# Performance work log

Measured on AMD Instinct MI355X. Metric: run time of the kernel, lower is better.

Reference implementation:

```python
import jax, jax.numpy as jnp
import numpy as np

NUM_SEGMENTS = 16

def setup_inputs() -> dict:
    key = jax.random.key(0)
    k1, k2, k3, k4 = jax.random.split(key, 4)
    C, R = 256, 4
    x = jax.random.normal(k1, (1000000, C), dtype=jnp.float32)
    indices = jax.random.randint(k2, (1000000,), 0, NUM_SEGMENTS, dtype=jnp.int64)
    # Linear weights (torch Linear: y = x @ W.T); store as (in, out) for einsum
    w1 = jax.random.normal(k3, (C, C // R), dtype=jnp.float32) / np.sqrt(C)
    w2 = jax.random.normal(k4, (C // R, C), dtype=jnp.float32) / np.sqrt(C // R)
    return {"x": x, "indices": indices, "w1": w1, "w2": w2}

def reference(x, indices, w1, w2):
    idx = indices.astype(jnp.int32)
    # scatter-mean over segments: (S, C)
    seg_sum = jax.ops.segment_sum(x, idx, num_segments=NUM_SEGMENTS)
    counts = jax.ops.segment_sum(jnp.ones((x.shape[0],), x.dtype), idx, num_segments=NUM_SEGMENTS)
    seg_mean = seg_sum / jnp.maximum(counts, 1.0)[:, None]
    # tiny SE MLP: Linear -> ReLU -> Linear -> Sigmoid
    h = jax.nn.relu(seg_mean @ w1)
    gate = jax.nn.sigmoid(h @ w2)  # (S, C)
    # gather per-point gate and modulate
    return x * gate[idx]
```

## Files before the change

### kernel.cpp

```cpp
#include <hip/hip_runtime.h>
#include <math.h>

#define C 256
#define S 16
#define CR 64
#define NREP 16

__global__ __launch_bounds__(256) void k_hist(
    const int* __restrict__ idx, int* __restrict__ pcnt, int nrows)
{
    const int lane = threadIdx.x & 63;
    const int tid  = blockIdx.x * blockDim.x + threadIdx.x;
    const int T    = gridDim.x * blockDim.x;
    const int padded = ((nrows + 63) >> 6) << 6;

    int c0=0,c1=0,c2=0,c3=0,c4=0,c5=0,c6=0,c7=0,
        c8=0,c9=0,c10=0,c11=0,c12=0,c13=0,c14=0,c15=0;

    for (int i = tid; i < padded; i += T) {
        const int v = (i < nrows) ? idx[i] : -1;
        #define CNT(K) c##K += (int)__popcll(__ballot(v == K));
        CNT(0)  CNT(1)  CNT(2)  CNT(3)  CNT(4)  CNT(5)  CNT(6)  CNT(7)
        CNT(8)  CNT(9)  CNT(10) CNT(11) CNT(12) CNT(13) CNT(14) CNT(15)
        #undef CNT
    }
    if (lane == 0) {
        #define FL(K) if (c##K) atomicAdd(&pcnt[K], c##K);
        FL(0)  FL(1)  FL(2)  FL(3)  FL(4)  FL(5)  FL(6)  FL(7)
        FL(8)  FL(9)  FL(10) FL(11) FL(12) FL(13) FL(14) FL(15)
        #undef FL
    }
}

__global__ __launch_bounds__(256, 2) void k_segsum(
    const float* __restrict__ x, const int* __restrict__ idx,
    float* __restrict__ psum, int nrows)
{
    const int lane = threadIdx.x & 63;
    const int w    = threadIdx.x >> 6;
    const int gw   = blockIdx.x * 4 + w;
    const int nw   = gridDim.x * 4;

    float4 a0={0,0,0,0},a1={0,0,0,0},a2={0,0,0,0},a3={0,0,0,0},
           a4={0,0,0,0},a5={0,0,0,0},a6={0,0,0,0},a7={0,0,0,0},
           a8={0,0,0,0},a9={0,0,0,0},a10={0,0,0,0},a11={0,0,0,0},
           a12={0,0,0,0},a13={0,0,0,0},a14={0,0,0,0},a15={0,0,0,0};

    const float4* __restrict__ x4 = reinterpret_cast<const float4*>(x);

    #define ACC1(K, sv, vv) { const float m = (sv == K) ? 1.0f : 0.0f; \
        a##K.x = fmaf(m, vv.x, a##K.x); a##K.y = fmaf(m, vv.y, a##K.y); \
        a##K.z = fmaf(m, vv.z, a##K.z); a##K.w = fmaf(m, vv.w, a##K.w); }
    #define ROW(sv, vv) \
        ACC1(0,sv,vv)  ACC1(1,sv,vv)  ACC1(2,sv,vv)  ACC1(3,sv,vv) \
        ACC1(4,sv,vv)  ACC1(5,sv,vv)  ACC1(6,sv,vv)  ACC1(7,sv,vv) \
        ACC1(8,sv,vv)  ACC1(9,sv,vv)  ACC1(10,sv,vv) ACC1(11,sv,vv) \
        ACC1(12,sv,vv) ACC1(13,sv,vv) ACC1(14,sv,vv) ACC1(15,sv,vv)

    const int nbatch = nrows >> 2;
    for (int b = gw; b < nbatch; b += nw) {
        const int r = b << 2;
        const int s0 = __builtin_amdgcn_readfirstlane(idx[r + 0]);
        const int s1 = __builtin_amdgcn_readfirstlane(idx[r + 1]);
        const int s2 = __builtin_amdgcn_readfirstlane(idx[r + 2]);
        const int s3 = __builtin_amdgcn_readfirstlane(idx[r + 3]);
        const float4* __restrict__ p = x4 + (size_t)r * (C/4) + lane;
        const float4 v0 = p[0 * (C/4)];
        const float4 v1 = p[1 * (C/4)];
        const float4 v2 = p[2 * (C/4)];
        const float4 v3 = p[3 * (C/4)];
        ROW(s0, v0) ROW(s1, v1) ROW(s2, v2) ROW(s3, v3)
    }
    if (gw == 0) {
        for (int r = nbatch << 2; r < nrows; ++r) {
            const int s = __builtin_amdgcn_readfirstlane(idx[r]);
            const float4 v = x4[(size_t)r * (C/4) + lane];
            ROW(s, v)
        }
    }
    #undef ROW
    #undef ACC1

    __shared__ float red[4][S][C];
    #define ST(K) *reinterpret_cast<float4*>(&red[w][K][4 * lane]) = a##K;
    ST(0)  ST(1)  ST(2)  ST(3)  ST(4)  ST(5)  ST(6)  ST(7)
    ST(8)  ST(9)  ST(10) ST(11) ST(12) ST(13) ST(14) ST(15)
    #undef ST
    __syncthreads();

    const int t   = threadIdx.x;
    const int rep = blockIdx.x & (NREP - 1);
    float* gs = psum + (size_t)rep * S * C;
    #pragma unroll
    for (int s_ = 0; s_ < S; s_++) {
        const float v = red[0][s_][t] + red[1][s_][t] +
                        red[2][s_][t] + red[3][s_][t];
        atomicAdd(&gs[s_ * C + t], v);
    }
}

__global__ __launch_bounds__(256) void k_mlp(
    const float* __restrict__ psum, const int* __restrict__ pcnt,
    const float* __restrict__ w1, const float* __restrict__ w2,
    float* __restrict__ gate)
{
    __shared__ float sm[S][C];
    __shared__ float h[S][CR];
    __shared__ float cnt[S];
    const int t = threadIdx.x;

    if (t < S) cnt[t] = fmaxf((float)pcnt[t], 1.0f);
    __syncthreads();

    for (int i = t; i < S * C; i += 256) {
        float v = 0.0f;
        #pragma unroll
        for (int r = 0; r < NREP; r++) v += psum[r * S * C + i];
        sm[i / C][i % C] = v / cnt[i / C];
    }
    __syncthreads();

    for (int o = t; o < S * CR; o += 256) {
        const int s = o / CR, j = o % CR;
        float acc = 0.0f;
        #pragma unroll 4
        for (int k = 0; k < C; k++) acc += sm[s][k] * w1[k * CR + j];
        h[s][j] = fmaxf(acc, 0.0f);
    }
    __syncthreads();

    for (int o = t; o < S * C; o += 256) {
        const int s = o / C, j = o % C;
        float acc = 0.0f;
        #pragma unroll
        for (int k = 0; k < CR; k++) acc += h[s][k] * w2[k * C + j];
        gate[o] = 1.0f / (1.0f + expf(-acc));
    }
}

__global__ __launch_bounds__(256) void k_mod(
    const float* __restrict__ x, const int* __restrict__ idx,
    const float* __restrict__ gate, float* __restrict__ out, int nrows)
{
    const int l    = threadIdx.x & 63;
    const int wrow = threadIdx.x >> 6;
    const float4* __restrict__ x4 = reinterpret_cast<const float4*>(x);
    const float4* __restrict__ g4 = reinterpret_cast<const float4*>(gate);
    float4* __restrict__ o4 = reinterpret_cast<float4*>(out);

    for (int row = blockIdx.x * 4 + wrow; row < nrows; row += gridDim.x * 4) {
        const int s = idx[row];
        float4 v = x4[row * (C / 4) + l];
        const float4 g = g4[s * (C / 4) + l];
        v.x *= g.x; v.y *= g.y; v.z *= g.z; v.w *= g.w;
        o4[row * (C / 4) + l] = v;
    }
}

extern "C" void kernel_launch(void* const* d_in, const int* in_sizes, int n_in,
                              void* d_out, int out_size, void* d_ws, size_t ws_size,
                              hipStream_t stream)
{
    const float* x   = (const float*)d_in[0];
    const int*   idx = (const int*)  d_in[1];
    const float* w1  = (const float*)d_in[2];
    const float* w2  = (const float*)d_in[3];
    float* out = (float*)d_out;
    const int nrows = in_sizes[1];

    float* psum = (float*)d_ws;
    int*   pcnt = (int*)(psum + NREP * S * C);
    float* gate = (float*)(pcnt + S);

    const size_t zero_bytes = NREP * S * C * sizeof(float) + S * sizeof(int);
    hipMemsetAsync(d_ws, 0, zero_bytes, stream);

    k_hist  <<<  64, 256, 0, stream>>>(idx, pcnt, nrows);
    k_segsum<<<1024, 256, 0, stream>>>(x, idx, psum, nrows);
    k_mlp   <<<   1, 256, 0, stream>>>(psum, pcnt, w1, w2, gate);
    k_mod   <<<2048, 256, 0, stream>>>(x, idx, gate, out, nrows);
}
```

Baseline: 740.2 us.

## Batch rows per wave with lane-broadcast indices and nontemporal loads/stores

Both the segment-sum and modulate kernels now give each wave a 64-row superblock. The wave loads all 64 indices with one coalesced load and broadcasts each one with readlane, and it issues several row loads at a time as nontemporal accesses to raise memory-level parallelism. The segsum kernel halves its shared reduction buffer by reducing in two 8-segment passes and raises its occupancy hint to 4 blocks per SM. The histogram grid doubles. More waves per SM may raise register pressure or cause spills with 64 accumulator floats, and nontemporal loads keep x out of cache between the two passes.

```diff
diff --git a/kernel.cpp b/kernel.cpp
--- a/kernel.cpp
+++ b/kernel.cpp
@@ -5,6 +5,8 @@
 #define S 16
 #define CR 64
 #define NREP 16
+
+typedef float f4 __attribute__((ext_vector_type(4)));
 
 __global__ __launch_bounds__(256) void k_hist(
     const int* __restrict__ idx, int* __restrict__ pcnt, int nrows)
@@ -32,7 +34,7 @@
     }
 }
 
-__global__ __launch_bounds__(256, 2) void k_segsum(
+__global__ __launch_bounds__(256, 4) void k_segsum(
     const float* __restrict__ x, const int* __restrict__ idx,
     float* __restrict__ psum, int nrows)
 {
@@ -41,12 +43,12 @@
     const int gw   = blockIdx.x * 4 + w;
     const int nw   = gridDim.x * 4;
 
-    float4 a0={0,0,0,0},a1={0,0,0,0},a2={0,0,0,0},a3={0,0,0,0},
-           a4={0,0,0,0},a5={0,0,0,0},a6={0,0,0,0},a7={0,0,0,0},
-           a8={0,0,0,0},a9={0,0,0,0},a10={0,0,0,0},a11={0,0,0,0},
-           a12={0,0,0,0},a13={0,0,0,0},a14={0,0,0,0},a15={0,0,0,0};
-
-    const float4* __restrict__ x4 = reinterpret_cast<const float4*>(x);
+    f4 a0={0,0,0,0},a1={0,0,0,0},a2={0,0,0,0},a3={0,0,0,0},
+       a4={0,0,0,0},a5={0,0,0,0},a6={0,0,0,0},a7={0,0,0,0},
+       a8={0,0,0,0},a9={0,0,0,0},a10={0,0,0,0},a11={0,0,0,0},
+       a12={0,0,0,0},a13={0,0,0,0},a14={0,0,0,0},a15={0,0,0,0};
+
+    const f4* __restrict__ x4 = reinterpret_cast<const f4*>(x);
 
     #define ACC1(K, sv, vv) { const float m = (sv == K) ? 1.0f : 0.0f; \
         a##K.x = fmaf(m, vv.x, a##K.x); a##K.y = fmaf(m, vv.y, a##K.y); \
@@ -57,46 +59,59 @@
         ACC1(8,sv,vv)  ACC1(9,sv,vv)  ACC1(10,sv,vv) ACC1(11,sv,vv) \
         ACC1(12,sv,vv) ACC1(13,sv,vv) ACC1(14,sv,vv) ACC1(15,sv,vv)
 
-    const int nbatch = nrows >> 2;
-    for (int b = gw; b < nbatch; b += nw) {
-        const int r = b << 2;
-        const int s0 = __builtin_amdgcn_readfirstlane(idx[r + 0]);
-        const int s1 = __builtin_amdgcn_readfirstlane(idx[r + 1]);
-        const int s2 = __builtin_amdgcn_readfirstlane(idx[r + 2]);
-        const int s3 = __builtin_amdgcn_readfirstlane(idx[r + 3]);
-        const float4* __restrict__ p = x4 + (size_t)r * (C/4) + lane;
-        const float4 v0 = p[0 * (C/4)];
-        const float4 v1 = p[1 * (C/4)];
-        const float4 v2 = p[2 * (C/4)];
-        const float4 v3 = p[3 * (C/4)];
-        ROW(s0, v0) ROW(s1, v1) ROW(s2, v2) ROW(s3, v3)
+    const int nsb = nrows >> 6;
+    for (int sb = gw; sb < nsb; sb += nw) {
+        const int row0 = sb << 6;
+        const int vidx = idx[row0 + lane];
+        const f4* __restrict__ p = x4 + (size_t)row0 * (C/4) + lane;
+        #pragma unroll 1
+        for (int j = 0; j < 64; j += 8) {
+            f4  v[8];
+            int s[8];
+            #pragma unroll
+            for (int k = 0; k < 8; k++)
+                v[k] = __builtin_nontemporal_load(&p[(size_t)(j + k) * (C/4)]);
+            #pragma unroll
+            for (int k = 0; k < 8; k++)
+                s[k] = __builtin_amdgcn_readlane(vidx, j + k);
+            #pragma unroll
+            for (int k = 0; k < 8; k++) { ROW(s[k], v[k]) }
+        }
     }
     if (gw == 0) {
-        for (int r = nbatch << 2; r < nrows; ++r) {
-            const int s = __builtin_amdgcn_readfirstlane(idx[r]);
-            const float4 v = x4[(size_t)r * (C/4) + lane];
-            ROW(s, v)
+        for (int r = nsb << 6; r < nrows; ++r) {
+            const int sv = __builtin_amdgcn_readfirstlane(idx[r]);
+            const f4 vv = x4[(size_t)r * (C/4) + lane];
+            ROW(sv, vv)
         }
     }
     #undef ROW
     #undef ACC1
 
-    __shared__ float red[4][S][C];
-    #define ST(K) *reinterpret_cast<float4*>(&red[w][K][4 * lane]) = a##K;
-    ST(0)  ST(1)  ST(2)  ST(3)  ST(4)  ST(5)  ST(6)  ST(7)
-    ST(8)  ST(9)  ST(10) ST(11) ST(12) ST(13) ST(14) ST(15)
-    #undef ST
-    __syncthreads();
-
+    __shared__ float red[4][8][C];
     const int t   = threadIdx.x;
     const int rep = blockIdx.x & (NREP - 1);
     float* gs = psum + (size_t)rep * S * C;
+
+    #define ST(K, SL) *reinterpret_cast<f4*>(&red[w][SL][4 * lane]) = a##K;
+    ST(0,0) ST(1,1) ST(2,2) ST(3,3) ST(4,4) ST(5,5) ST(6,6) ST(7,7)
+    __syncthreads();
     #pragma unroll
-    for (int s_ = 0; s_ < S; s_++) {
+    for (int s_ = 0; s_ < 8; s_++) {
         const float v = red[0][s_][t] + red[1][s_][t] +
                         red[2][s_][t] + red[3][s_][t];
         atomicAdd(&gs[s_ * C + t], v);
     }
+    __syncthreads();
+    ST(8,0) ST(9,1) ST(10,2) ST(11,3) ST(12,4) ST(13,5) ST(14,6) ST(15,7)
+    __syncthreads();
+    #pragma unroll
+    for (int s_ = 0; s_ < 8; s_++) {
+        const float v = red[0][s_][t] + red[1][s_][t] +
+                        red[2][s_][t] + red[3][s_][t];
+        atomicAdd(&gs[(8 + s_) * C + t], v);
+    }
+    #undef ST
 }
 
 __global__ __launch_bounds__(256) void k_mlp(
@@ -142,18 +157,49 @@
     const float* __restrict__ x, const int* __restrict__ idx,
     const float* __restrict__ gate, float* __restrict__ out, int nrows)
 {
-    const int l    = threadIdx.x & 63;
-    const int wrow = threadIdx.x >> 6;
-    const float4* __restrict__ x4 = reinterpret_cast<const float4*>(x);
-    const float4* __restrict__ g4 = reinterpret_cast<const float4*>(gate);
-    float4* __restrict__ o4 = reinterpret_cast<float4*>(out);
-
-    for (int row = blockIdx.x * 4 + wrow; row < nrows; row += gridDim.x * 4) {
-        const int s = idx[row];
-        float4 v = x4[row * (C / 4) + l];
-        const float4 g = g4[s * (C / 4) + l];
-        v.x *= g.x; v.y *= g.y; v.z *= g.z; v.w *= g.w;
-        o4[row * (C / 4) + l] = v;
+    const int lane = threadIdx.x & 63;
+    const int w    = threadIdx.x >> 6;
+    const int gw   = blockIdx.x * 4 + w;
+    const int nw   = gridDim.x * 4;
+    const f4* __restrict__ x4 = reinterpret_cast<const f4*>(x);
+    const f4* __restrict__ g4 = reinterpret_cast<const f4*>(gate);
+    f4* __restrict__ o4 = reinterpret_cast<f4*>(out);
+
+    const int nsb = nrows >> 6;
+    for (int sb = gw; sb < nsb; sb += nw) {
+        const int row0 = sb << 6;
+        const int vidx = idx[row0 + lane];
+        const f4* __restrict__ p = x4 + (size_t)row0 * (C/4) + lane;
+        f4* __restrict__ q = o4 + (size_t)row0 * (C/4) + lane;
+        #pragma unroll 1
+        for (int j = 0; j < 64; j += 4) {
+            const int s0 = __builtin_amdgcn_readlane(vidx, j + 0);
+            const int s1 = __builtin_amdgcn_readlane(vidx, j + 1);
+            const int s2 = __builtin_amdgcn_readlane(vidx, j + 2);
+            const int s3 = __builtin_amdgcn_readlane(vidx, j + 3);
+            f4 v0 = __builtin_nontemporal_load(&p[(size_t)(j+0) * (C/4)]);
+            f4 v1 = __builtin_nontemporal_load(&p[(size_t)(j+1) * (C/4)]);
+            f4 v2 = __builtin_nontemporal_load(&p[(size_t)(j+2) * (C/4)]);
+            f4 v3 = __builtin_nontemporal_load(&p[(size_t)(j+3) * (C/4)]);
+            const f4 g0 = g4[s0 * (C/4) + lane];
+            const f4 g1 = g4[s1 * (C/4) + lane];
+            const f4 g2 = g4[s2 * (C/4) + lane];
+            const f4 g3 = g4[s3 * (C/4) + lane];
+            v0 *= g0; v1 *= g1; v2 *= g2; v3 *= g3;
+            __builtin_nontemporal_store(v0, &q[(size_t)(j+0) * (C/4)]);
+            __builtin_nontemporal_store(v1, &q[(size_t)(j+1) * (C/4)]);
+            __builtin_nontemporal_store(v2, &q[(size_t)(j+2) * (C/4)]);
+            __builtin_nontemporal_store(v3, &q[(size_t)(j+3) * (C/4)]);
+        }
+    }
+    if (gw == 0) {
+        for (int r = nsb << 6; r < nrows; ++r) {
+            const int s = idx[r];
+            f4 v = x4[(size_t)r * (C/4) + lane];
+            const f4 g = g4[s * (C/4) + lane];
+            v *= g;
+            o4[(size_t)r * (C/4) + lane] = v;
+        }
     }
 }
 
@@ -173,9 +219,9 @@
     float* gate = (float*)(pcnt + S);
 
     const size_t zero_bytes = NREP * S * C * sizeof(float) + S * sizeof(int);
-    hipMemsetAsync(d_ws, 0, zero_bytes, stream);
-
-    k_hist  <<<  64, 256, 0, stream>>>(idx, pcnt, nrows);
+    (void)hipMemsetAsync(d_ws, 0, zero_bytes, stream);
+
+    k_hist  <<< 128, 256, 0, stream>>>(idx, pcnt, nrows);
     k_segsum<<<1024, 256, 0, stream>>>(x, idx, psum, nrows);
     k_mlp   <<<   1, 256, 0, stream>>>(psum, pcnt, w1, w2, gate);
     k_mod   <<<2048, 256, 0, stream>>>(x, idx, gate, out, nrows);
```

Result: no change. 748.2 us (+1.1%).

## Flatten segment-sum loop to element grid-stride and halve LDS for higher occupancy

Applied to the files above, without the earlier changes.

The segment-sum kernel now walks x as a flat float4 grid-stride stream, two elements per iteration, with each lane loading its row index directly. It no longer assigns four rows per wave with scalar readfirstlane indices. The block-level LDS reduction buffer is halved and reused for two passes over the 16 segments. Together with launch bounds raised to 4 blocks per CU, this aims for more resident waves to hide memory latency. The histogram grid is also doubled. In exchange, each wave keeps fewer independent loads in flight, segment comparisons move from scalar to vector registers, and the reduction adds an extra barrier.

```diff
diff --git a/kernel.cpp b/kernel.cpp
--- a/kernel.cpp
+++ b/kernel.cpp
@@ -5,6 +5,8 @@
 #define S 16
 #define CR 64
 #define NREP 16
+
+typedef float f4 __attribute__((ext_vector_type(4)));
 
 __global__ __launch_bounds__(256) void k_hist(
     const int* __restrict__ idx, int* __restrict__ pcnt, int nrows)
@@ -32,21 +34,20 @@
     }
 }
 
-__global__ __launch_bounds__(256, 2) void k_segsum(
+__global__ __launch_bounds__(256, 4) void k_segsum(
     const float* __restrict__ x, const int* __restrict__ idx,
     float* __restrict__ psum, int nrows)
 {
-    const int lane = threadIdx.x & 63;
-    const int w    = threadIdx.x >> 6;
-    const int gw   = blockIdx.x * 4 + w;
-    const int nw   = gridDim.x * 4;
+    const int  tid = blockIdx.x * 256 + threadIdx.x;
+    const int  T   = gridDim.x * 256;
+    const long n4  = (long)nrows * (C / 4);
 
-    float4 a0={0,0,0,0},a1={0,0,0,0},a2={0,0,0,0},a3={0,0,0,0},
-           a4={0,0,0,0},a5={0,0,0,0},a6={0,0,0,0},a7={0,0,0,0},
-           a8={0,0,0,0},a9={0,0,0,0},a10={0,0,0,0},a11={0,0,0,0},
-           a12={0,0,0,0},a13={0,0,0,0},a14={0,0,0,0},a15={0,0,0,0};
+    f4 a0={0,0,0,0},a1={0,0,0,0},a2={0,0,0,0},a3={0,0,0,0},
+       a4={0,0,0,0},a5={0,0,0,0},a6={0,0,0,0},a7={0,0,0,0},
+       a8={0,0,0,0},a9={0,0,0,0},a10={0,0,0,0},a11={0,0,0,0},
+       a12={0,0,0,0},a13={0,0,0,0},a14={0,0,0,0},a15={0,0,0,0};
 
-    const float4* __restrict__ x4 = reinterpret_cast<const float4*>(x);
+    const f4* __restrict__ x4 = reinterpret_cast<const f4*>(x);
 
     #define ACC1(K, sv, vv) { const float m = (sv == K) ? 1.0f : 0.0f; \
         a##K.x = fmaf(m, vv.x, a##K.x); a##K.y = fmaf(m, vv.y, a##K.y); \
@@ -57,46 +58,49 @@
         ACC1(8,sv,vv)  ACC1(9,sv,vv)  ACC1(10,sv,vv) ACC1(11,sv,vv) \
         ACC1(12,sv,vv) ACC1(13,sv,vv) ACC1(14,sv,vv) ACC1(15,sv,vv)
 
-    const int nbatch = nrows >> 2;
-    for (int b = gw; b < nbatch; b += nw) {
-        const int r = b << 2;
-        const int s0 = __builtin_amdgcn_readfirstlane(idx[r + 0]);
-        const int s1 = __builtin_amdgcn_readfirstlane(idx[r + 1]);
-        const int s2 = __builtin_amdgcn_readfirstlane(idx[r + 2]);
-        const int s3 = __builtin_amdgcn_readfirstlane(idx[r + 3]);
-        const float4* __restrict__ p = x4 + (size_t)r * (C/4) + lane;
-        const float4 v0 = p[0 * (C/4)];
-        const float4 v1 = p[1 * (C/4)];
-        const float4 v2 = p[2 * (C/4)];
-        const float4 v3 = p[3 * (C/4)];
-        ROW(s0, v0) ROW(s1, v1) ROW(s2, v2) ROW(s3, v3)
+    long i = tid;
+    for (; i + T < n4; i += 2L * T) {
+        const f4  v0 = x4[i];
+        const f4  v1 = x4[i + T];
+        const int s0 = idx[i >> 6];
+        const int s1 = idx[(i + T) >> 6];
+        ROW(s0, v0)
+        ROW(s1, v1)
     }
-    if (gw == 0) {
-        for (int r = nbatch << 2; r < nrows; ++r) {
-            const int s = __builtin_amdgcn_readfirstlane(idx[r]);
-            const float4 v = x4[(size_t)r * (C/4) + lane];
-            ROW(s, v)
-        }
+    for (; i < n4; i += T) {
+        const f4  v = x4[i];
+        const int s = idx[i >> 6];
+        ROW(s, v)
     }
     #undef ROW
     #undef ACC1
 
-    __shared__ float red[4][S][C];
-    #define ST(K) *reinterpret_cast<float4*>(&red[w][K][4 * lane]) = a##K;
-    ST(0)  ST(1)  ST(2)  ST(3)  ST(4)  ST(5)  ST(6)  ST(7)
-    ST(8)  ST(9)  ST(10) ST(11) ST(12) ST(13) ST(14) ST(15)
-    #undef ST
+    __shared__ float red[4][8][C];
+    const int w    = threadIdx.x >> 6;
+    const int lane = threadIdx.x & 63;
+    const int t    = threadIdx.x;
+    const int rep  = blockIdx.x & (NREP - 1);
+    float* gs = psum + (size_t)rep * S * C;
+
+    #define ST(K, SL) *reinterpret_cast<f4*>(&red[w][SL][4 * lane]) = a##K;
+    ST(0,0) ST(1,1) ST(2,2) ST(3,3) ST(4,4) ST(5,5) ST(6,6) ST(7,7)
     __syncthreads();
-
-    const int t   = threadIdx.x;
-    const int rep = blockIdx.x & (NREP - 1);
-    float* gs = psum + (size_t)rep * S * C;
     #pragma unroll
-    for (int s_ = 0; s_ < S; s_++) {
+    for (int s_ = 0; s_ < 8; s_++) {
         const float v = red[0][s_][t] + red[1][s_][t] +
                         red[2][s_][t] + red[3][s_][t];
         atomicAdd(&gs[s_ * C + t], v);
     }
+    __syncthreads();
+    ST(8,0) ST(9,1) ST(10,2) ST(11,3) ST(12,4) ST(13,5) ST(14,6) ST(15,7)
+    __syncthreads();
+    #pragma unroll
+    for (int s_ = 0; s_ < 8; s_++) {
+        const float v = red[0][s_][t] + red[1][s_][t] +
+                        red[2][s_][t] + red[3][s_][t];
+        atomicAdd(&gs[(8 + s_) * C + t], v);
+    }
+    #undef ST
 }
 
 __global__ __launch_bounds__(256) void k_mlp(
@@ -173,9 +177,9 @@
     float* gate = (float*)(pcnt + S);
 
     const size_t zero_bytes = NREP * S * C * sizeof(float) + S * sizeof(int);
-    hipMemsetAsync(d_ws, 0, zero_bytes, stream);
+    (void)hipMemsetAsync(d_ws, 0, zero_bytes, stream);
 
-    k_hist  <<<  64, 256, 0, stream>>>(idx, pcnt, nrows);
+    k_hist  <<< 128, 256, 0, stream>>>(idx, pcnt, nrows);
     k_segsum<<<1024, 256, 0, stream>>>(x, idx, psum, nrows);
     k_mlp   <<<   1, 256, 0, stream>>>(psum, pcnt, w1, w2, gate);
     k_mod   <<<2048, 256, 0, stream>>>(x, idx, gate, out, nrows);
```

Measured after the change: 794.3 us. 7.3% more time.
